# Kernel tuning notes

Measured on AMD Instinct MI355X. Metric: run time of the kernel, lower is better.

The kernel has to match this reference:

```python
import jax, jax.numpy as jnp
import numpy as np
import math

B, T, TE, D, H = 1, 2048, 1024, 1024, 16
HD = D // H
INF = 1e9  # infinity_proxy from the original module
INIT_SCALE = 0.02


def sinusoid_pos_emb(timesteps, dim):
    # Transformer-XL sinusoids for relative positions [timesteps-1 .. 0].
    inv_freq = 1.0 / (10000.0 ** (np.arange(0, dim, 2) / dim))
    pos_seq = np.arange(timesteps - 1, -1, -1.0)
    inp = np.einsum('i,j->ij', pos_seq, inv_freq)
    return np.concatenate([np.sin(inp), np.cos(inp)], axis=-1).astype(np.float32)


def relative_shift(x):
    # x: [b, h, t, T] -> TXL left-pad / reshape / slice shift trick.
    b, h, t1, t2 = x.shape
    x = jnp.pad(x, ((0, 0), (0, 0), (0, 0), (1, 0)))
    x = x.reshape(b, h, t2 + 1, t1)[:, :, 1:, :]
    return x.reshape(b, h, t1, t2)


def setup_inputs() -> dict:
    key = jax.random.key(0)
    ks = jax.random.split(key, 12)
    s = INIT_SCALE
    x = jax.random.normal(ks[0], (B, T, D), jnp.float32)
    extra = jax.random.normal(ks[1], (B, TE, D), jnp.float32)
    # causal mask over the in-sequence keys; full visibility on the extra memory
    mask = jnp.broadcast_to(jnp.tril(jnp.ones((T, T), jnp.float32))[None, None], (B, 1, T, T))
    extra_mask = jnp.ones((B, 1, T, TE), jnp.float32)
    Wq = jax.random.normal(ks[2], (D, D), jnp.float32) * s
    Wk = jax.random.normal(ks[3], (D, D), jnp.float32) * s
    Wv = jax.random.normal(ks[4], (D, D), jnp.float32) * s
    Wek = jax.random.normal(ks[5], (D, D), jnp.float32) * s
    Wev = jax.random.normal(ks[6], (D, D), jnp.float32) * s
    Wr = jax.random.normal(ks[7], (D, D), jnp.float32) * s
    Wo = jax.random.normal(ks[8], (D, D), jnp.float32) * s
    r_w_bias = jax.random.normal(ks[9], (H, HD), jnp.float32) * s
    r_r_bias = jax.random.normal(ks[10], (H, HD), jnp.float32) * s
    return dict(x=x, extra=extra, mask=mask, extra_mask=extra_mask,
                Wq=Wq, Wk=Wk, Wv=Wv, Wek=Wek, Wev=Wev, Wr=Wr, Wo=Wo,
                r_w_bias=r_w_bias, r_r_bias=r_r_bias)


def reference(x, extra, mask, extra_mask, Wq, Wk, Wv, Wek, Wev, Wr, Wo, r_w_bias, r_r_bias):
    b, t, d = x.shape
    te = extra.shape[1]
    # conv1d(kernel=1, no bias) == matmul projections; cache_steps=0 so y == x
    q = (x @ Wq).reshape(b, t, H, HD)
    k = (x @ Wk).reshape(b, t, H, HD)
    v = (x @ Wv).reshape(b, t, H, HD)
    # Transformer-XL relative-position attend_fn
    pos = jnp.asarray(sinusoid_pos_emb(t, d))            # [t, D]
    r = (pos @ Wr).reshape(t, H, HD)                      # [t, H, HD]
    content = jnp.einsum('bthd,bThd->bhtT', q + r_w_bias, k)
    rel = relative_shift(jnp.einsum('bthd,Thd->bhtT', q + r_r_bias, r))
    attn = content + rel
    attn = attn * mask - INF * (1.0 - mask)
    # extra keys/values use plain dot-product attention (no rel-pos)
    ek = (extra @ Wek).reshape(b, te, H, HD)
    ev = (extra @ Wev).reshape(b, te, H, HD)
    eattn = jnp.einsum('bthd,bThd->bhtT', q, ek)
    eattn = eattn * extra_mask - INF * (1.0 - extra_mask)
    attn = jnp.concatenate([attn, eattn], axis=-1) * (1.0 / math.sqrt(HD))
    p = jax.nn.softmax(attn, axis=-1)
    vv = jnp.concatenate([v, ev], axis=1)                 # [b, t+te, H, HD]
    out = jnp.einsum('bhtT,bThd->bthd', p, vv).reshape(b, t, d)
    return out @ Wo  # final conv1d, with_final_bias=False
```

## Files before the change

### kernel.cpp

```cpp
#include <hip/hip_runtime.h>
#include <hip/hip_bf16.h>
#include <math.h>

#define T_LEN 2048
#define TE_LEN 1024
#define D_DIM 1024
#define H_NUM 16
#define HD_DIM 64
#define R_PAD 64

typedef unsigned short ushort;
typedef __attribute__((ext_vector_type(8))) short short8;
typedef __attribute__((ext_vector_type(4))) float f32x4;
typedef __attribute__((ext_vector_type(4))) ushort ushort4v;

__device__ __forceinline__ ushort f2b(float f) {
    unsigned u = __builtin_bit_cast(unsigned, f);
    u += 0x7fffu + ((u >> 16) & 1u);
    return (ushort)(u >> 16);
}
__device__ __forceinline__ float b2f(ushort s) {
    unsigned u = ((unsigned)s) << 16;
    return __builtin_bit_cast(float, u);
}

__device__ __forceinline__ void gld16(const ushort* g, ushort* l) {
    __builtin_amdgcn_global_load_lds(
        (const __attribute__((address_space(1))) unsigned int*)g,
        (__attribute__((address_space(3))) unsigned int*)l, 16, 0, 0);
}

union U8 { short8 v; ushort u[8]; };

__global__ void prep_kernel(const float* __restrict__ x, const float* __restrict__ extra,
                            ushort* __restrict__ pos, ushort* __restrict__ xb,
                            ushort* __restrict__ eb) {
    const int q = blockIdx.x * 256 + threadIdx.x;
    const int PQ = 524288;
    const int XQ = 1048576;
    if (q < PQ) {
        int idx = q * 4;
        int i = idx >> 10, j = idx & 1023;
        bool sinreg = (j < 512);
        int jj = sinreg ? j : j - 512;
        float p = (float)(2047 - i);
        ushort4v o;
#pragma unroll
        for (int u = 0; u < 4; u++) {
            float inv = exp2f((float)(jj + u) * -0.025952563241f);
            float fa = p * inv;
            ((ushort*)&o)[u] = f2b(sinreg ? sinf(fa) : cosf(fa));
        }
        *(ushort4v*)&pos[idx] = o;
    } else if (q < XQ) {
        int idx = (q - PQ) * 4;
        float4 v = *(const float4*)&x[idx];
        ushort4v o = {f2b(v.x), f2b(v.y), f2b(v.z), f2b(v.w)};
        *(ushort4v*)&xb[idx] = o;
    } else {
        int idx = (q - XQ) * 4;
        float4 v = *(const float4*)&extra[idx];
        ushort4v o = {f2b(v.x), f2b(v.y), f2b(v.z), f2b(v.w)};
        *(ushort4v*)&eb[idx] = o;
    }
}

__global__ __launch_bounds__(256) void transpose7_kernel(
    const float* __restrict__ W0, const float* __restrict__ W1,
    const float* __restrict__ W2, const float* __restrict__ W3,
    const float* __restrict__ W4, const float* __restrict__ W5,
    const float* __restrict__ W6, ushort* __restrict__ out) {
    const float* Ws[7] = {W0, W1, W2, W3, W4, W5, W6};
    const float* W = Ws[blockIdx.z];
    ushort* WT = out + (size_t)blockIdx.z * (1024 * 1024);
    __shared__ float tile[32][33];
    int c0 = blockIdx.x * 32, r0 = blockIdx.y * 32;
    int tid = threadIdx.x;
#pragma unroll
    for (int p = 0; p < 4; p++) {
        int idx = tid + p * 256;
        int r = idx >> 5, c = idx & 31;
        tile[r][c] = W[(size_t)(r0 + r) * D_DIM + c0 + c];
    }
    __syncthreads();
#pragma unroll
    for (int p = 0; p < 4; p++) {
        int idx = tid + p * 256;
        int r = idx >> 5, c = idx & 31;
        WT[(size_t)(c0 + r) * D_DIM + r0 + c] = f2b(tile[c][r]);
    }
}

__global__ __launch_bounds__(256) void gemm_mega(
    const ushort* __restrict__ xb, const ushort* __restrict__ posb,
    const ushort* __restrict__ eb, const ushort* __restrict__ WT,
    ushort* __restrict__ Qb, ushort* __restrict__ Kb, ushort* __restrict__ VTb,
    ushort* __restrict__ Rb, ushort* __restrict__ EKb, ushort* __restrict__ EVTb) {
    __shared__ ushort As[128 * 72];
    __shared__ ushort Bs[128 * 72];
    const int tid = threadIdx.x;
    const int lane = tid & 63, w = tid >> 6;
    const int l15 = lane & 15, quad = lane >> 4;
    const int wm = w & 1, wn = w >> 1;
    const size_t M1 = 1024 * 1024;

    int idx = blockIdx.x;
    const ushort *A, *BT;
    ushort* dst;
    int m0, nb0, nc0, ldt = 1024;
    bool transp = false;
    if (idx < 384) {
        m0 = (idx & 15) * 128; nb0 = (idx >> 4) * 128;
        A = xb; BT = WT;
        nc0 = nb0 & 1023;
        int seg = nb0 >> 10;
        if (seg == 0) dst = Qb;
        else if (seg == 1) dst = Kb;
        else { dst = VTb; transp = true; ldt = T_LEN; }
    } else if (idx < 512) {
        int i = idx - 384;
        m0 = (i & 15) * 128; nb0 = (i >> 4) * 128; nc0 = nb0;
        A = posb; BT = WT + 5 * M1; dst = Rb;
    } else {
        int i = idx - 512;
        m0 = (i & 7) * 128; nb0 = (i >> 3) * 128; nc0 = nb0 & 1023;
        A = eb; BT = WT + 3 * M1;
        if (nb0 < 1024) dst = EKb;
        else { dst = EVTb; transp = true; ldt = TE_LEN; }
    }

    f32x4 acc[16];
#pragma unroll
    for (int i = 0; i < 16; i++) acc[i] = (f32x4){0.f, 0.f, 0.f, 0.f};

    for (int k0 = 0; k0 < 1024; k0 += 64) {
#pragma unroll
        for (int p = 0; p < 4; p++) {
            int lin = tid + p * 256;
            int r = lin >> 3, c = (lin & 7) * 8;
            *(short8*)&As[r * 72 + c] = *(const short8*)&A[(size_t)(m0 + r) * 1024 + k0 + c];
            *(short8*)&Bs[r * 72 + c] = *(const short8*)&BT[(size_t)(nb0 + r) * 1024 + k0 + c];
        }
        __syncthreads();
#pragma unroll
        for (int kc = 0; kc < 2; kc++) {
            short8 bfr[4];
#pragma unroll
            for (int nf = 0; nf < 4; nf++)
                bfr[nf] = *(const short8*)&Bs[(wn * 64 + nf * 16 + l15) * 72 + kc * 32 + quad * 8];
#pragma unroll
            for (int mf = 0; mf < 4; mf++) {
                short8 afr = *(const short8*)&As[(wm * 64 + mf * 16 + l15) * 72 + kc * 32 + quad * 8];
#pragma unroll
                for (int nf = 0; nf < 4; nf++)
                    acc[mf * 4 + nf] = __builtin_amdgcn_mfma_f32_16x16x32_bf16(afr, bfr[nf], acc[mf * 4 + nf], 0, 0, 0);
            }
        }
        __syncthreads();
    }

#pragma unroll
    for (int mf = 0; mf < 4; mf++) {
#pragma unroll
        for (int nf = 0; nf < 4; nf++) {
            f32x4 a = acc[mf * 4 + nf];
            const int mrow = m0 + wm * 64 + mf * 16 + quad * 4;
            const int nc = nc0 + wn * 64 + nf * 16 + l15;
            if (transp) {
                ushort4v v = {f2b(a[0]), f2b(a[1]), f2b(a[2]), f2b(a[3])};
                *(ushort4v*)&dst[(size_t)nc * ldt + mrow] = v;
            } else {
#pragma unroll
                for (int r = 0; r < 4; r++) dst[(size_t)(mrow + r) * 1024 + nc] = f2b(a[r]);
            }
        }
    }
}

__global__ __launch_bounds__(256) void gemm_wo(const ushort* __restrict__ A,
                                               const ushort* __restrict__ BT,
                                               float* __restrict__ out) {
    __shared__ ushort As[128 * 72];
    __shared__ ushort Bs[64 * 72];
    const int tid = threadIdx.x;
    const int lane = tid & 63, w = tid >> 6;
    const int l15 = lane & 15, quad = lane >> 4;
    const int wm = w & 1, wn = w >> 1;
    const int m0 = blockIdx.y * 128, n0 = blockIdx.x * 64;

    f32x4 acc[8];
#pragma unroll
    for (int i = 0; i < 8; i++) acc[i] = (f32x4){0.f, 0.f, 0.f, 0.f};

    for (int k0 = 0; k0 < 1024; k0 += 64) {
#pragma unroll
        for (int p = 0; p < 4; p++) {
            int lin = tid + p * 256;
            int r = lin >> 3, c = (lin & 7) * 8;
            *(short8*)&As[r * 72 + c] = *(const short8*)&A[(size_t)(m0 + r) * 1024 + k0 + c];
        }
#pragma unroll
        for (int p = 0; p < 2; p++) {
            int lin = tid + p * 256;
            int r = lin >> 3, c = (lin & 7) * 8;
            *(short8*)&Bs[r * 72 + c] = *(const short8*)&BT[(size_t)(n0 + r) * 1024 + k0 + c];
        }
        __syncthreads();
#pragma unroll
        for (int kc = 0; kc < 2; kc++) {
            short8 bfr[2];
#pragma unroll
            for (int nf = 0; nf < 2; nf++)
                bfr[nf] = *(const short8*)&Bs[(wn * 32 + nf * 16 + l15) * 72 + kc * 32 + quad * 8];
#pragma unroll
            for (int mf = 0; mf < 4; mf++) {
                short8 afr = *(const short8*)&As[(wm * 64 + mf * 16 + l15) * 72 + kc * 32 + quad * 8];
#pragma unroll
                for (int nf = 0; nf < 2; nf++)
                    acc[mf * 2 + nf] = __builtin_amdgcn_mfma_f32_16x16x32_bf16(afr, bfr[nf], acc[mf * 2 + nf], 0, 0, 0);
            }
        }
        __syncthreads();
    }

#pragma unroll
    for (int mf = 0; mf < 4; mf++) {
#pragma unroll
        for (int nf = 0; nf < 2; nf++) {
            f32x4 a = acc[mf * 2 + nf];
            const int mrow = m0 + wm * 64 + mf * 16 + quad * 4;
            const int nc = n0 + wn * 32 + nf * 16 + l15;
#pragma unroll
            for (int r = 0; r < 4; r++) out[(size_t)(mrow + r) * 1024 + nc] = a[r];
        }
    }
}

__global__ __launch_bounds__(256) void attn_kernel(
    const ushort* __restrict__ Qb, const ushort* __restrict__ Kb,
    const ushort* __restrict__ VT, const ushort* __restrict__ Rb,
    const ushort* __restrict__ EKb, const ushort* __restrict__ EVT,
    const float* __restrict__ rwb, const float* __restrict__ rrb,
    ushort* __restrict__ AOb) {
    __shared__ ushort Kst[2][64 * 64];
    __shared__ ushort Vst[2][64 * 64];
    __shared__ ushort Rst[2][128 * 64];
    __shared__ ushort Plds[4][16 * 72];

    const int tid = threadIdx.x;
    const int lane = tid & 63, w = tid >> 6;
    const int l15 = lane & 15, quad = lane >> 4;
    const int blk = blockIdx.x;
    const int xcd = blk & 7, rnd = blk >> 8, slot = (blk >> 3) & 31;
    const int h = xcd * 2 + rnd;
    const int qt = rnd ? slot : 31 - slot;
    const int t0 = qt * 64, tf = t0 + w * 16;
    const int hbase = h * HD_DIM;

    short8 qw[2], qr[2], qp[2];
#pragma unroll
    for (int kh = 0; kh < 2; kh++) {
        int dof = hbase + kh * 32 + quad * 8;
        U8 raw; raw.v = *(const short8*)&Qb[(size_t)(tf + l15) * D_DIM + dof];
        U8 a, b, c;
#pragma unroll
        for (int j = 0; j < 8; j++) {
            float f = b2f(raw.u[j]);
            a.u[j] = f2b((f + rwb[dof + j]) * 0.125f);
            b.u[j] = f2b((f + rrb[dof + j]) * 0.125f);
            c.u[j] = f2b(f * 0.125f);
        }
        qw[kh] = a.v; qr[kh] = b.v; qp[kh] = c.v;
    }

    float lr[4] = {0.f, 0.f, 0.f, 0.f};
    f32x4 O[4];
#pragma unroll
    for (int i = 0; i < 4; i++) O[i] = (f32x4){0.f, 0.f, 0.f, 0.f};

    const int nin = qt + 1, ntot = nin + 16;

    auto stage = [&](int tt2, int buf) {
        const bool ins = tt2 < nin;
        const int j0 = ins ? tt2 * 64 : (tt2 - nin) * 64;
        const ushort* ksrc = ins ? Kb : EKb;
        const ushort* vsrc = ins ? VT : EVT;
        const int ldv = ins ? T_LEN : TE_LEN;
#pragma unroll
        for (int i = 0; i < 2; i++) {
            int ci = w * 128 + i * 64 + lane;
            int row = ci >> 3, c = (ci & 7) ^ (row & 7);
            gld16(ksrc + (size_t)(j0 + row) * 1024 + hbase + c * 8, &Kst[buf][(w * 128 + i * 64) * 8]);
            gld16(vsrc + (size_t)(hbase + row) * ldv + j0 + c * 8, &Vst[buf][(w * 128 + i * 64) * 8]);
        }
        if (ins) {
            const int U0B = 1984 - t0 + j0;
#pragma unroll
            for (int i = 0; i < 4; i++) {
                int ci = w * 256 + i * 64 + lane;
                int row = ci >> 3, c = (ci & 7) ^ (row & 7);
                gld16(Rb + (size_t)(U0B + row) * 1024 + hbase + c * 8, &Rst[buf][(w * 256 + i * 64) * 8]);
            }
        }
    };

    int srcA[4]; bool lowcA[4];
#pragma unroll
    for (int r = 0; r < 4; r++) {
        const int m = quad * 4 + r;
        const int cb = 15 - m + l15;
        srcA[r] = (lane & 48) | (cb & 15);
        lowcA[r] = (cb < 16);
    }
    const int rbase = 48 - 16 * w;

    stage(0, 0);

#pragma unroll 1
    for (int tt = 0; tt < ntot; tt++) {
        const int b = tt & 1;
        __syncthreads();
        if (tt + 1 < ntot) stage(tt + 1, 1 - b);

        const bool ins = tt < nin;
        const int j0 = ins ? tt * 64 : 0;

        f32x4 con[4];
#pragma unroll
        for (int i = 0; i < 4; i++) con[i] = (f32x4){0.f, 0.f, 0.f, 0.f};
#pragma unroll
        for (int kh = 0; kh < 2; kh++) {
            const short8* qa = ins ? &qw[kh] : &qp[kh];
#pragma unroll
            for (int nh = 0; nh < 4; nh++) {
                const int row = nh * 16 + l15;
                short8 kf = *(const short8*)&Kst[b][(row * 8 + ((kh * 4 + quad) ^ (l15 & 7))) * 8];
                con[nh] = __builtin_amdgcn_mfma_f32_16x16x32_bf16(*qa, kf, con[nh], 0, 0, 0);
            }
        }

        if (ins) {
            f32x4 rel[5];
#pragma unroll
            for (int i = 0; i < 5; i++) rel[i] = (f32x4){0.f, 0.f, 0.f, 0.f};
#pragma unroll
            for (int kh = 0; kh < 2; kh++)
#pragma unroll
                for (int cf = 0; cf < 5; cf++) {
                    const int rrow = rbase + cf * 16 + l15;
                    short8 rf = *(const short8*)&Rst[b][(rrow * 8 + ((kh * 4 + quad) ^ (l15 & 7))) * 8];
                    rel[cf] = __builtin_amdgcn_mfma_f32_16x16x32_bf16(qr[kh], rf, rel[cf], 0, 0, 0);
                }
            const bool needmask = (tt == nin - 1);
#pragma unroll
            for (int r = 0; r < 4; r++) {
                const int m = quad * 4 + r;
                float b0 = __shfl(rel[0][r], srcA[r]);
                float b1 = __shfl(rel[1][r], srcA[r]);
                float b2 = __shfl(rel[2][r], srcA[r]);
                float b3 = __shfl(rel[3][r], srcA[r]);
                float b4 = __shfl(rel[4][r], srcA[r]);
                float rv0 = lowcA[r] ? b0 : b1, rv1 = lowcA[r] ? b1 : b2;
                float rv2 = lowcA[r] ? b2 : b3, rv3 = lowcA[r] ? b3 : b4;
                float p0 = __expf(con[0][r] + rv0);
                float p1 = __expf(con[1][r] + rv1);
                float p2 = __expf(con[2][r] + rv2);
                float p3 = __expf(con[3][r] + rv3);
                if (needmask) {
                    const int t = tf + m;
                    if (j0 + l15 > t)      p0 = 0.f;
                    if (j0 + 16 + l15 > t) p1 = 0.f;
                    if (j0 + 32 + l15 > t) p2 = 0.f;
                    if (j0 + 48 + l15 > t) p3 = 0.f;
                }
                lr[r] += (p0 + p1) + (p2 + p3);
                Plds[w][m * 72 + l15]      = f2b(p0);
                Plds[w][m * 72 + 16 + l15] = f2b(p1);
                Plds[w][m * 72 + 32 + l15] = f2b(p2);
                Plds[w][m * 72 + 48 + l15] = f2b(p3);
            }
        } else {
#pragma unroll
            for (int r = 0; r < 4; r++) {
                const int m = quad * 4 + r;
                float p0 = __expf(con[0][r]);
                float p1 = __expf(con[1][r]);
                float p2 = __expf(con[2][r]);
                float p3 = __expf(con[3][r]);
                lr[r] += (p0 + p1) + (p2 + p3);
                Plds[w][m * 72 + l15]      = f2b(p0);
                Plds[w][m * 72 + 16 + l15] = f2b(p1);
                Plds[w][m * 72 + 32 + l15] = f2b(p2);
                Plds[w][m * 72 + 48 + l15] = f2b(p3);
            }
        }

#pragma unroll
        for (int kc = 0; kc < 2; kc++) {
            short8 pa = *(const short8*)&Plds[w][l15 * 72 + kc * 32 + quad * 8];
#pragma unroll
            for (int df = 0; df < 4; df++) {
                const int row = df * 16 + l15;
                short8 vb = *(const short8*)&Vst[b][(row * 8 + ((kc * 4 + quad) ^ (l15 & 7))) * 8];
                O[df] = __builtin_amdgcn_mfma_f32_16x16x32_bf16(pa, vb, O[df], 0, 0, 0);
            }
        }
    }

#pragma unroll
    for (int r = 0; r < 4; r++) {
#pragma unroll
        for (int dd = 1; dd < 16; dd <<= 1) lr[r] += __shfl_xor(lr[r], dd);
        const float inv = 1.0f / lr[r];
#pragma unroll
        for (int df = 0; df < 4; df++)
            AOb[(size_t)(tf + quad * 4 + r) * D_DIM + hbase + df * 16 + l15] = f2b(O[df][r] * inv);
    }
}

extern "C" void kernel_launch(void* const* d_in, const int* in_sizes, int n_in,
                              void* d_out, int out_size, void* d_ws, size_t ws_size,
                              hipStream_t stream) {
    const float* x     = (const float*)d_in[0];
    const float* extra = (const float*)d_in[1];
    const float* Wq  = (const float*)d_in[4];
    const float* Wk  = (const float*)d_in[5];
    const float* Wv  = (const float*)d_in[6];
    const float* Wek = (const float*)d_in[7];
    const float* Wev = (const float*)d_in[8];
    const float* Wr  = (const float*)d_in[9];
    const float* Wo  = (const float*)d_in[10];
    const float* rwb = (const float*)d_in[11];
    const float* rrb = (const float*)d_in[12];
    float* out = (float*)d_out;

    ushort* ws = (ushort*)d_ws;
    const size_t M1 = 1024 * 1024;
    size_t o = 0;
    ushort* posb = ws + o; o += 2 * M1;
    ushort* xb   = ws + o; o += 2 * M1;
    ushort* eb   = ws + o; o += M1;
    ushort* WT   = ws + o; o += 7 * M1;
    ushort* Qb   = ws + o; o += 2 * M1;
    ushort* Kb   = ws + o; o += 2 * M1;
    ushort* VTb  = ws + o; o += 2 * M1;
    ushort* Rb   = ws + o; o += (size_t)(T_LEN + R_PAD) * 1024;
    ushort* EKb  = ws + o; o += M1;
    ushort* EVTb = ws + o; o += M1;
    ushort* AOb  = posb;

    prep_kernel<<<5120, 256, 0, stream>>>(x, extra, posb, xb, eb);
    transpose7_kernel<<<dim3(32, 32, 7), 256, 0, stream>>>(Wq, Wk, Wv, Wek, Wev, Wr, Wo, WT);

    hipMemsetAsync(Rb + (size_t)T_LEN * 1024, 0, (size_t)R_PAD * 1024 * sizeof(ushort), stream);

    gemm_mega<<<640, 256, 0, stream>>>(xb, posb, eb, WT, Qb, Kb, VTb, Rb, EKb, EVTb);

    attn_kernel<<<512, 256, 0, stream>>>(Qb, Kb, VTb, Rb, EKb, EVTb, rwb, rrb, AOb);

    gemm_wo<<<dim3(16, 16), 256, 0, stream>>>(AOb, WT + 6 * M1, out);
}
```

Before: 278.4 us.

## Shrink attention KV tiles to 32, ring-buffer R, async swizzled GEMM loads

The attention kernel now walks keys in 32-wide tiles instead of 64. The relative-position R tile lives in a single 128-row ring buffer, so each step stages only 32 new R rows rather than reloading 128 rows per tile. This cuts LDS footprint and redundant R traffic, and masks only the diagonal tiles, but it doubles the number of loop iterations and barriers. The projection and output GEMMs switch to direct global-to-LDS loads into an XOR-swizzled layout in place of padded register staging, and the R-padding memset is folded into the transpose launch to drop one API call.

```diff
diff --git a/kernel.cpp b/kernel.cpp
--- a/kernel.cpp
+++ b/kernel.cpp
@@ -69,7 +69,16 @@
     const float* __restrict__ W0, const float* __restrict__ W1,
     const float* __restrict__ W2, const float* __restrict__ W3,
     const float* __restrict__ W4, const float* __restrict__ W5,
-    const float* __restrict__ W6, ushort* __restrict__ out) {
+    const float* __restrict__ W6, ushort* __restrict__ out,
+    ushort* __restrict__ Rpad) {
+    if (blockIdx.z == 7) {
+        int gid = (blockIdx.y * 32 + blockIdx.x) * 256 + threadIdx.x;
+        if (gid < (R_PAD * 1024) / 8) {
+            short8 z = {0, 0, 0, 0, 0, 0, 0, 0};
+            *(short8*)&Rpad[gid * 8] = z;
+        }
+        return;
+    }
     const float* Ws[7] = {W0, W1, W2, W3, W4, W5, W6};
     const float* W = Ws[blockIdx.z];
     ushort* WT = out + (size_t)blockIdx.z * (1024 * 1024);
@@ -96,8 +105,8 @@
     const ushort* __restrict__ eb, const ushort* __restrict__ WT,
     ushort* __restrict__ Qb, ushort* __restrict__ Kb, ushort* __restrict__ VTb,
     ushort* __restrict__ Rb, ushort* __restrict__ EKb, ushort* __restrict__ EVTb) {
-    __shared__ ushort As[128 * 72];
-    __shared__ ushort Bs[128 * 72];
+    __shared__ ushort As[128 * 64];
+    __shared__ ushort Bs[128 * 64];
     const int tid = threadIdx.x;
     const int lane = tid & 63, w = tid >> 6;
     const int l15 = lane & 15, quad = lane >> 4;
@@ -134,29 +143,32 @@
     for (int i = 0; i < 16; i++) acc[i] = (f32x4){0.f, 0.f, 0.f, 0.f};
 
     for (int k0 = 0; k0 < 1024; k0 += 64) {
-#pragma unroll
-        for (int p = 0; p < 4; p++) {
-            int lin = tid + p * 256;
-            int r = lin >> 3, c = (lin & 7) * 8;
-            *(short8*)&As[r * 72 + c] = *(const short8*)&A[(size_t)(m0 + r) * 1024 + k0 + c];
-            *(short8*)&Bs[r * 72 + c] = *(const short8*)&BT[(size_t)(nb0 + r) * 1024 + k0 + c];
+        __syncthreads();
+#pragma unroll
+        for (int i = 0; i < 4; i++) {
+            int ci = i * 256 + tid;
+            int row = ci >> 3, cs = (ci & 7) ^ (row & 7);
+            gld16(A + (size_t)(m0 + row) * 1024 + k0 + cs * 8, &As[(i * 32 + w * 8) * 64]);
+            gld16(BT + (size_t)(nb0 + row) * 1024 + k0 + cs * 8, &Bs[(i * 32 + w * 8) * 64]);
         }
         __syncthreads();
 #pragma unroll
         for (int kc = 0; kc < 2; kc++) {
             short8 bfr[4];
 #pragma unroll
-            for (int nf = 0; nf < 4; nf++)
-                bfr[nf] = *(const short8*)&Bs[(wn * 64 + nf * 16 + l15) * 72 + kc * 32 + quad * 8];
+            for (int nf = 0; nf < 4; nf++) {
+                const int row = wn * 64 + nf * 16 + l15;
+                bfr[nf] = *(const short8*)&Bs[(row * 8 + ((kc * 4 + quad) ^ (row & 7))) * 8];
+            }
 #pragma unroll
             for (int mf = 0; mf < 4; mf++) {
-                short8 afr = *(const short8*)&As[(wm * 64 + mf * 16 + l15) * 72 + kc * 32 + quad * 8];
+                const int row = wm * 64 + mf * 16 + l15;
+                short8 afr = *(const short8*)&As[(row * 8 + ((kc * 4 + quad) ^ (row & 7))) * 8];
 #pragma unroll
                 for (int nf = 0; nf < 4; nf++)
                     acc[mf * 4 + nf] = __builtin_amdgcn_mfma_f32_16x16x32_bf16(afr, bfr[nf], acc[mf * 4 + nf], 0, 0, 0);
             }
         }
-        __syncthreads();
     }
 
 #pragma unroll
@@ -180,8 +192,8 @@
 __global__ __launch_bounds__(256) void gemm_wo(const ushort* __restrict__ A,
                                                const ushort* __restrict__ BT,
                                                float* __restrict__ out) {
-    __shared__ ushort As[128 * 72];
-    __shared__ ushort Bs[64 * 72];
+    __shared__ ushort As[128 * 64];
+    __shared__ ushort Bs[64 * 64];
     const int tid = threadIdx.x;
     const int lane = tid & 63, w = tid >> 6;
     const int l15 = lane & 15, quad = lane >> 4;
@@ -193,34 +205,37 @@
     for (int i = 0; i < 8; i++) acc[i] = (f32x4){0.f, 0.f, 0.f, 0.f};
 
     for (int k0 = 0; k0 < 1024; k0 += 64) {
-#pragma unroll
-        for (int p = 0; p < 4; p++) {
-            int lin = tid + p * 256;
-            int r = lin >> 3, c = (lin & 7) * 8;
-            *(short8*)&As[r * 72 + c] = *(const short8*)&A[(size_t)(m0 + r) * 1024 + k0 + c];
-        }
-#pragma unroll
-        for (int p = 0; p < 2; p++) {
-            int lin = tid + p * 256;
-            int r = lin >> 3, c = (lin & 7) * 8;
-            *(short8*)&Bs[r * 72 + c] = *(const short8*)&BT[(size_t)(n0 + r) * 1024 + k0 + c];
+        __syncthreads();
+#pragma unroll
+        for (int i = 0; i < 4; i++) {
+            int ci = i * 256 + tid;
+            int row = ci >> 3, cs = (ci & 7) ^ (row & 7);
+            gld16(A + (size_t)(m0 + row) * 1024 + k0 + cs * 8, &As[(i * 32 + w * 8) * 64]);
+        }
+#pragma unroll
+        for (int i = 0; i < 2; i++) {
+            int ci = i * 256 + tid;
+            int row = ci >> 3, cs = (ci & 7) ^ (row & 7);
+            gld16(BT + (size_t)(n0 + row) * 1024 + k0 + cs * 8, &Bs[(i * 32 + w * 8) * 64]);
         }
         __syncthreads();
 #pragma unroll
         for (int kc = 0; kc < 2; kc++) {
             short8 bfr[2];
 #pragma unroll
-            for (int nf = 0; nf < 2; nf++)
-                bfr[nf] = *(const short8*)&Bs[(wn * 32 + nf * 16 + l15) * 72 + kc * 32 + quad * 8];
+            for (int nf = 0; nf < 2; nf++) {
+                const int row = wn * 32 + nf * 16 + l15;
+                bfr[nf] = *(const short8*)&Bs[(row * 8 + ((kc * 4 + quad) ^ (row & 7))) * 8];
+            }
 #pragma unroll
             for (int mf = 0; mf < 4; mf++) {
-                short8 afr = *(const short8*)&As[(wm * 64 + mf * 16 + l15) * 72 + kc * 32 + quad * 8];
+                const int row = wm * 64 + mf * 16 + l15;
+                short8 afr = *(const short8*)&As[(row * 8 + ((kc * 4 + quad) ^ (row & 7))) * 8];
 #pragma unroll
                 for (int nf = 0; nf < 2; nf++)
                     acc[mf * 2 + nf] = __builtin_amdgcn_mfma_f32_16x16x32_bf16(afr, bfr[nf], acc[mf * 2 + nf], 0, 0, 0);
             }
         }
-        __syncthreads();
     }
 
 #pragma unroll
@@ -242,10 +257,10 @@
     const ushort* __restrict__ EKb, const ushort* __restrict__ EVT,
     const float* __restrict__ rwb, const float* __restrict__ rrb,
     ushort* __restrict__ AOb) {
-    __shared__ ushort Kst[2][64 * 64];
-    __shared__ ushort Vst[2][64 * 64];
-    __shared__ ushort Rst[2][128 * 64];
-    __shared__ ushort Plds[4][16 * 72];
+    __shared__ ushort Kst[2][32 * 64];
+    __shared__ ushort Vst[2][64 * 32];
+    __shared__ ushort Rst[128 * 64];
+    __shared__ ushort Plds[4][16 * 40];
 
     const int tid = threadIdx.x;
     const int lane = tid & 63, w = tid >> 6;
@@ -256,6 +271,7 @@
     const int qt = rnd ? slot : 31 - slot;
     const int t0 = qt * 64, tf = t0 + w * 16;
     const int hbase = h * HD_DIM;
+    const int base0 = 1984 - t0;
 
     short8 qw[2], qr[2], qp[2];
 #pragma unroll
@@ -278,31 +294,38 @@
 #pragma unroll
     for (int i = 0; i < 4; i++) O[i] = (f32x4){0.f, 0.f, 0.f, 0.f};
 
-    const int nin = qt + 1, ntot = nin + 16;
-
-    auto stage = [&](int tt2, int buf) {
+    const int nin = 2 * qt + 2, ntot = nin + 32;
+
+    auto stageKV = [&](int tt2, int buf) {
         const bool ins = tt2 < nin;
-        const int j0 = ins ? tt2 * 64 : (tt2 - nin) * 64;
+        const int j0 = ins ? tt2 * 32 : (tt2 - nin) * 32;
         const ushort* ksrc = ins ? Kb : EKb;
         const ushort* vsrc = ins ? VT : EVT;
         const int ldv = ins ? T_LEN : TE_LEN;
-#pragma unroll
-        for (int i = 0; i < 2; i++) {
-            int ci = w * 128 + i * 64 + lane;
-            int row = ci >> 3, c = (ci & 7) ^ (row & 7);
-            gld16(ksrc + (size_t)(j0 + row) * 1024 + hbase + c * 8, &Kst[buf][(w * 128 + i * 64) * 8]);
-            gld16(vsrc + (size_t)(hbase + row) * ldv + j0 + c * 8, &Vst[buf][(w * 128 + i * 64) * 8]);
-        }
-        if (ins) {
-            const int U0B = 1984 - t0 + j0;
-#pragma unroll
-            for (int i = 0; i < 4; i++) {
-                int ci = w * 256 + i * 64 + lane;
-                int row = ci >> 3, c = (ci & 7) ^ (row & 7);
-                gld16(Rb + (size_t)(U0B + row) * 1024 + hbase + c * 8, &Rst[buf][(w * 256 + i * 64) * 8]);
-            }
+        {
+            int row = tid >> 3, cs = (tid & 7) ^ (row & 7);
+            gld16(ksrc + (size_t)(j0 + row) * 1024 + hbase + cs * 8, &Kst[buf][w * 512]);
+        }
+        {
+            int row = tid >> 2, cs = (tid & 3) ^ (row & 3);
+            gld16(vsrc + (size_t)(hbase + row) * ldv + j0 + cs * 8, &Vst[buf][w * 512]);
         }
     };
+    auto stageR = [&](int slotbase, int rowbase) {
+        int k = tid >> 3;
+        int s = slotbase + k;
+        int cs = (tid & 7) ^ (s & 7);
+        gld16(Rb + (size_t)(rowbase + k) * 1024 + hbase + cs * 8,
+              &Rst[(slotbase + w * 8) * 64]);
+    };
+
+#pragma unroll
+    for (int i = 0; i < 3; i++) {
+        int ci = i * 256 + tid;
+        int k = ci >> 3, cs = (ci & 7) ^ (k & 7);
+        gld16(Rb + (size_t)(base0 + k) * 1024 + hbase + cs * 8, &Rst[(i * 32 + w * 8) * 64]);
+    }
+    stageKV(0, 0);
 
     int srcA[4]; bool lowcA[4];
 #pragma unroll
@@ -312,72 +335,63 @@
         srcA[r] = (lane & 48) | (cb & 15);
         lowcA[r] = (cb < 16);
     }
-    const int rbase = 48 - 16 * w;
-
-    stage(0, 0);
 
 #pragma unroll 1
     for (int tt = 0; tt < ntot; tt++) {
         const int b = tt & 1;
         __syncthreads();
-        if (tt + 1 < ntot) stage(tt + 1, 1 - b);
+        if (tt + 1 < ntot) {
+            stageKV(tt + 1, 1 - b);
+            if (tt + 1 < nin) stageR((96 + 32 * tt) & 127, base0 + 96 + 32 * tt);
+        }
 
         const bool ins = tt < nin;
-        const int j0 = ins ? tt * 64 : 0;
-
-        f32x4 con[4];
-#pragma unroll
-        for (int i = 0; i < 4; i++) con[i] = (f32x4){0.f, 0.f, 0.f, 0.f};
+        const int j0 = tt * 32;
+
+        f32x4 con[2];
+#pragma unroll
+        for (int i = 0; i < 2; i++) con[i] = (f32x4){0.f, 0.f, 0.f, 0.f};
 #pragma unroll
         for (int kh = 0; kh < 2; kh++) {
             const short8* qa = ins ? &qw[kh] : &qp[kh];
 #pragma unroll
-            for (int nh = 0; nh < 4; nh++) {
+            for (int nh = 0; nh < 2; nh++) {
                 const int row = nh * 16 + l15;
-                short8 kf = *(const short8*)&Kst[b][(row * 8 + ((kh * 4 + quad) ^ (l15 & 7))) * 8];
+                short8 kf = *(const short8*)&Kst[b][(row * 8 + ((kh * 4 + quad) ^ (row & 7))) * 8];
                 con[nh] = __builtin_amdgcn_mfma_f32_16x16x32_bf16(*qa, kf, con[nh], 0, 0, 0);
             }
         }
 
         if (ins) {
-            f32x4 rel[5];
-#pragma unroll
-            for (int i = 0; i < 5; i++) rel[i] = (f32x4){0.f, 0.f, 0.f, 0.f};
+            f32x4 rel[3];
+#pragma unroll
+            for (int i = 0; i < 3; i++) rel[i] = (f32x4){0.f, 0.f, 0.f, 0.f};
 #pragma unroll
             for (int kh = 0; kh < 2; kh++)
 #pragma unroll
-                for (int cf = 0; cf < 5; cf++) {
-                    const int rrow = rbase + cf * 16 + l15;
-                    short8 rf = *(const short8*)&Rst[b][(rrow * 8 + ((kh * 4 + quad) ^ (l15 & 7))) * 8];
+                for (int cf = 0; cf < 3; cf++) {
+                    const int s = (48 - 16 * w + 32 * tt + 16 * cf + l15) & 127;
+                    short8 rf = *(const short8*)&Rst[(s * 8 + ((kh * 4 + quad) ^ (s & 7))) * 8];
                     rel[cf] = __builtin_amdgcn_mfma_f32_16x16x32_bf16(qr[kh], rf, rel[cf], 0, 0, 0);
                 }
-            const bool needmask = (tt == nin - 1);
+            const bool needmask = (j0 + 31 > tf);
 #pragma unroll
             for (int r = 0; r < 4; r++) {
                 const int m = quad * 4 + r;
                 float b0 = __shfl(rel[0][r], srcA[r]);
                 float b1 = __shfl(rel[1][r], srcA[r]);
                 float b2 = __shfl(rel[2][r], srcA[r]);
-                float b3 = __shfl(rel[3][r], srcA[r]);
-                float b4 = __shfl(rel[4][r], srcA[r]);
                 float rv0 = lowcA[r] ? b0 : b1, rv1 = lowcA[r] ? b1 : b2;
-                float rv2 = lowcA[r] ? b2 : b3, rv3 = lowcA[r] ? b3 : b4;
                 float p0 = __expf(con[0][r] + rv0);
                 float p1 = __expf(con[1][r] + rv1);
-                float p2 = __expf(con[2][r] + rv2);
-                float p3 = __expf(con[3][r] + rv3);
                 if (needmask) {
                     const int t = tf + m;
                     if (j0 + l15 > t)      p0 = 0.f;
                     if (j0 + 16 + l15 > t) p1 = 0.f;
-                    if (j0 + 32 + l15 > t) p2 = 0.f;
-                    if (j0 + 48 + l15 > t) p3 = 0.f;
                 }
-                lr[r] += (p0 + p1) + (p2 + p3);
-                Plds[w][m * 72 + l15]      = f2b(p0);
-                Plds[w][m * 72 + 16 + l15] = f2b(p1);
-                Plds[w][m * 72 + 32 + l15] = f2b(p2);
-                Plds[w][m * 72 + 48 + l15] = f2b(p3);
+                lr[r] += p0 + p1;
+                Plds[w][m * 40 + l15]      = f2b(p0);
+                Plds[w][m * 40 + 16 + l15] = f2b(p1);
             }
         } else {
 #pragma unroll
@@ -385,25 +399,18 @@
                 const int m = quad * 4 + r;
                 float p0 = __expf(con[0][r]);
                 float p1 = __expf(con[1][r]);
-                float p2 = __expf(con[2][r]);
-                float p3 = __expf(con[3][r]);
-                lr[r] += (p0 + p1) + (p2 + p3);
-                Plds[w][m * 72 + l15]      = f2b(p0);
-                Plds[w][m * 72 + 16 + l15] = f2b(p1);
-                Plds[w][m * 72 + 32 + l15] = f2b(p2);
-                Plds[w][m * 72 + 48 + l15] = f2b(p3);
-            }
-        }
-
-#pragma unroll
-        for (int kc = 0; kc < 2; kc++) {
-            short8 pa = *(const short8*)&Plds[w][l15 * 72 + kc * 32 + quad * 8];
-#pragma unroll
-            for (int df = 0; df < 4; df++) {
-                const int row = df * 16 + l15;
-                short8 vb = *(const short8*)&Vst[b][(row * 8 + ((kc * 4 + quad) ^ (l15 & 7))) * 8];
-                O[df] = __builtin_amdgcn_mfma_f32_16x16x32_bf16(pa, vb, O[df], 0, 0, 0);
-            }
+                lr[r] += p0 + p1;
+                Plds[w][m * 40 + l15]      = f2b(p0);
+                Plds[w][m * 40 + 16 + l15] = f2b(p1);
+            }
+        }
+
+        short8 pa = *(const short8*)&Plds[w][l15 * 40 + quad * 8];
+#pragma unroll
+        for (int df = 0; df < 4; df++) {
+            const int row = df * 16 + l15;
+            short8 vb = *(const short8*)&Vst[b][(row * 4 + (quad ^ (row & 3))) * 8];
+            O[df] = __builtin_amdgcn_mfma_f32_16x16x32_bf16(pa, vb, O[df], 0, 0, 0);
         }
     }
 
@@ -450,9 +457,8 @@
     ushort* AOb  = posb;
 
     prep_kernel<<<5120, 256, 0, stream>>>(x, extra, posb, xb, eb);
-    transpose7_kernel<<<dim3(32, 32, 7), 256, 0, stream>>>(Wq, Wk, Wv, Wek, Wev, Wr, Wo, WT);
-
-    hipMemsetAsync(Rb + (size_t)T_LEN * 1024, 0, (size_t)R_PAD * 1024 * sizeof(ushort), stream);
+    transpose7_kernel<<<dim3(32, 32, 8), 256, 0, stream>>>(
+        Wq, Wk, Wv, Wek, Wev, Wr, Wo, WT, Rb + (size_t)T_LEN * 1024);
 
     gemm_mega<<<640, 256, 0, stream>>>(xb, posb, eb, WT, Qb, Kb, VTb, Rb, EKb, EVTb);
 
```

Measured after the change: 277.2 us. Within noise of the previous version (-0.4%).
